# Performance work log

Hardware: AMD Instinct MI355X
Metric: run time of the kernel (lower is better)

Reference implementation:

```python
import jax, jax.numpy as jnp
import numpy as np

N_NODES = 200000
N_HYPEREDGES = 50000
NNZ = 3200000
D = 128
LEAKY = 0.2


def setup_inputs() -> dict:
    key = jax.random.key(0)
    k1, k2, k3, k4 = jax.random.split(key, 4)
    embs = jax.random.normal(k1, (N_NODES, D), dtype=jnp.float32)
    vals = jax.random.uniform(k2, (NNZ,), dtype=jnp.float32)
    rows = jax.random.randint(k3, (NNZ,), 0, N_NODES, dtype=jnp.int32)
    cols = jax.random.randint(k4, (NNZ,), 0, N_HYPEREDGES, dtype=jnp.int32)
    return {
        "embs": embs,
        "vals": vals,
        "rows": rows,
        "cols": cols,
        "n_nodes": N_NODES,
        "n_hyperedges": N_HYPEREDGES,
    }


def reference(embs, vals, rows, cols, n_nodes, n_hyperedges):
    # adj is sparse COO: adj[rows[k], cols[k]] = vals[k], shape [n_nodes, n_hyperedges]
    # Step 1: he = adj.T @ embs  -> [n_hyperedges, D]
    he = jax.ops.segment_sum(embs[rows] * vals[:, None], cols,
                             num_segments=n_hyperedges)
    # Step 2: out = adj @ he     -> [n_nodes, D]
    out = jax.ops.segment_sum(he[cols] * vals[:, None], rows,
                              num_segments=n_nodes)
    # LeakyReLU(negative_slope=LEAKY)
    return jnp.where(out >= 0, out, LEAKY * out)
```

## Files before the change

kernel.cpp:

```cpp
#include <hip/hip_runtime.h>

#define DIM 128
#define LEAKY 0.2f
#define N_NODES_C 200000
#define N_HE_C 50000

#define NNZ_SLAB 2048
#define SEGC_PB 64
#define NB_C 782
#define SEGR_PB 256
#define NB_R 782
#define CAP_B 4608

typedef float f32x4 __attribute__((ext_vector_type(4)));

__device__ __forceinline__ unsigned bf16r(float f) {
    return (__float_as_uint(f) + 0x8000u) >> 16;
}
__device__ __forceinline__ float bf16lo(unsigned u) {
    return __uint_as_float((u & 0xFFFFu) << 16);
}
__device__ __forceinline__ float bf16hi(unsigned u) {
    return __uint_as_float(u & 0xFFFF0000u);
}

__global__ void convert_bf16(const f32x4* __restrict__ in, uint2* __restrict__ out, int n4) {
    int t = blockIdx.x * blockDim.x + threadIdx.x;
    if (t >= n4) return;
    f32x4 x = __builtin_nontemporal_load(in + t);
    out[t] = make_uint2((bf16r(x.y) << 16) | bf16r(x.x),
                        (bf16r(x.w) << 16) | bf16r(x.z));
}

__global__ void __launch_bounds__(256)
bin_append(const int* __restrict__ rows, const int* __restrict__ cols,
           const float* __restrict__ vals, int nnz,
           int* __restrict__ curC, int* __restrict__ curR,
           int2* __restrict__ stagC, int2* __restrict__ stagR) {
    __shared__ int sr[NNZ_SLAB];
    __shared__ int sc[NNZ_SLAB];
    __shared__ int sv[NNZ_SLAB];
    __shared__ int cnt[NB_C + NB_R];
    for (int i = threadIdx.x; i < NB_C + NB_R; i += 256) cnt[i] = 0;
    __syncthreads();
    int base = blockIdx.x * NNZ_SLAB;
    int nloc = nnz - base; if (nloc > NNZ_SLAB) nloc = NNZ_SLAB;
    for (int i = threadIdx.x; i < nloc; i += 256) {
        int k = base + i;
        int r = rows[k], c = cols[k];
        sr[i] = r; sc[i] = c; sv[i] = __float_as_int(vals[k]);
        atomicAdd(&cnt[c >> 6], 1);
        atomicAdd(&cnt[NB_C + (r >> 8)], 1);
    }
    __syncthreads();
    for (int i = threadIdx.x; i < NB_C; i += 256) {
        int n = cnt[i];
        cnt[i] = n ? atomicAdd(&curC[i], n) : 0;
    }
    for (int i = threadIdx.x; i < NB_R; i += 256) {
        int n = cnt[NB_C + i];
        cnt[NB_C + i] = n ? atomicAdd(&curR[i], n) : 0;
    }
    __syncthreads();
    for (int i = threadIdx.x; i < nloc; i += 256) {
        int r = sr[i], c = sc[i], v = sv[i];
        int bc = c >> 6;
        int oc = atomicAdd(&cnt[bc], 1);
        if (oc < CAP_B)
            stagC[(size_t)bc * CAP_B + oc] = make_int2(((c & 63) << 18) | r, v);
        int br = r >> 8;
        int orr = atomicAdd(&cnt[NB_C + br], 1);
        if (orr < CAP_B)
            stagR[(size_t)br * CAP_B + orr] = make_int2(((r & 255) << 16) | c, v);
    }
}

template <int SEG_PB, int LSHIFT, int MODE>
__global__ void __launch_bounds__(256)
bucket_sort(const int* __restrict__ cur, const int2* __restrict__ stag,
            unsigned* __restrict__ outPacked,
            int* __restrict__ startOut, int* __restrict__ endOut, int nseg) {
    __shared__ int2 ent[CAP_B];
    __shared__ int cnt[SEG_PB];
    __shared__ int scn[SEG_PB];
    int b = blockIdx.x;
    size_t lo = (size_t)b * CAP_B;
    int n = cur[b]; if (n > CAP_B) n = CAP_B;
    int t = threadIdx.x;
    for (int i = t; i < SEG_PB; i += 256) cnt[i] = 0;
    __syncthreads();
    for (int i = t; i < n; i += 256) {
        int2 e = stag[lo + i];
        ent[i] = e;
        atomicAdd(&cnt[e.x >> LSHIFT], 1);
    }
    __syncthreads();
    if (t < SEG_PB) scn[t] = cnt[t];
    __syncthreads();
    for (int off = 1; off < SEG_PB; off <<= 1) {
        int x = (t < SEG_PB) ? scn[t] : 0;
        int add = (t >= off && t < SEG_PB) ? scn[t - off] : 0;
        __syncthreads();
        if (t < SEG_PB) scn[t] = x + add;
        __syncthreads();
    }
    int segBase = b * SEG_PB;
    if (t < SEG_PB) {
        int excl = t ? scn[t - 1] : 0;
        if (segBase + t < nseg) {
            startOut[segBase + t] = (int)lo + excl;
            endOut[segBase + t]   = (int)lo + scn[t];
        }
        cnt[t] = excl;
    }
    __syncthreads();
    for (int i = t; i < n; i += 256) {
        int2 e = ent[i];
        int s = e.x >> LSHIFT;
        int pos = (int)lo + atomicAdd(&cnt[s], 1);
        unsigned w;
        if (MODE == 0) {
            unsigned v14 = ((unsigned)e.y + 0x10000u) >> 17;
            w = ((unsigned)(e.x & 0x3FFFF) << 14) | (v14 & 0x3FFFu);
        } else {
            unsigned vb = ((unsigned)e.y + 0x8000u) >> 16;
            w = ((unsigned)(e.x & 0xFFFF) << 16) | vb;
        }
        outPacked[pos] = w;
    }
}


__global__ void seg_pass1(const int* __restrict__ start, const int* __restrict__ end,
                          const unsigned* __restrict__ packed,
                          const unsigned* __restrict__ srcb, unsigned* __restrict__ dstb,
                          int nseg) {
    int wid = (int)((blockIdx.x * (unsigned)blockDim.x + threadIdx.x) >> 6);
    int lane = threadIdx.x & 63;
    if (wid >= nseg) return;
    int s = start[wid];
    int e = end[wid];
    float ax = 0.f, ay = 0.f;
    int j = s;
    for (; j + 8 <= e; j += 8) {
        #pragma unroll
        for (int u = 0; u < 8; ++u) {
            unsigned p = packed[j + u];
            unsigned w = srcb[(size_t)(p >> 14) * 64 + lane];
            float v = __uint_as_float((p & 0x3FFFu) << 17);
            ax += bf16lo(w) * v;
            ay += bf16hi(w) * v;
        }
    }
    for (; j < e; ++j) {
        unsigned p = packed[j];
        unsigned w = srcb[(size_t)(p >> 14) * 64 + lane];
        float v = __uint_as_float((p & 0x3FFFu) << 17);
        ax += bf16lo(w) * v;
        ay += bf16hi(w) * v;
    }
    dstb[(size_t)wid * 64 + lane] = (bf16r(ay) << 16) | bf16r(ax);
}

__global__ void seg_pass2(const int* __restrict__ start, const int* __restrict__ end,
                          const unsigned* __restrict__ packed,
                          const unsigned* __restrict__ srcb, float* __restrict__ dst,
                          int nseg) {
    int wid = (int)((blockIdx.x * (unsigned)blockDim.x + threadIdx.x) >> 6);
    int lane = threadIdx.x & 63;
    if (wid >= nseg) return;
    int s = start[wid];
    int e = end[wid];
    float ax = 0.f, ay = 0.f;
    int j = s;
    for (; j + 4 <= e; j += 4) {
        #pragma unroll
        for (int u = 0; u < 4; ++u) {
            unsigned p = packed[j + u];
            unsigned w = srcb[(size_t)(p >> 16) * 64 + lane];
            float v = __uint_as_float(p << 16);
            ax += bf16lo(w) * v;
            ay += bf16hi(w) * v;
        }
    }
    for (; j < e; ++j) {
        unsigned p = packed[j];
        unsigned w = srcb[(size_t)(p >> 16) * 64 + lane];
        float v = __uint_as_float(p << 16);
        ax += bf16lo(w) * v;
        ay += bf16hi(w) * v;
    }
    ax = ax >= 0.f ? ax : LEAKY * ax;
    ay = ay >= 0.f ? ay : LEAKY * ay;
    unsigned long long bits = ((unsigned long long)__float_as_uint(ay) << 32) |
                              (unsigned long long)__float_as_uint(ax);
    __builtin_nontemporal_store(bits,
        reinterpret_cast<unsigned long long*>(dst) + (size_t)wid * 64 + lane);
}

__global__ void scatter_step(const float* __restrict__ src, const float* __restrict__ vals,
                             const int* __restrict__ gidx, const int* __restrict__ sidx,
                             float* __restrict__ dst, int nnz) {
    long long t = (long long)blockIdx.x * blockDim.x + threadIdx.x;
    int k = (int)(t >> 5);
    if (k >= nnz) return;
    int q = ((int)t & 31) << 2;
    int g = gidx[k];
    int s = sidx[k];
    float v = vals[k];
    const float4 e = *reinterpret_cast<const float4*>(src + (size_t)g * DIM + q);
    float* dp = dst + (size_t)s * DIM + q;
    unsafeAtomicAdd(dp + 0, e.x * v);
    unsafeAtomicAdd(dp + 1, e.y * v);
    unsafeAtomicAdd(dp + 2, e.z * v);
    unsafeAtomicAdd(dp + 3, e.w * v);
}

__global__ void leaky_inplace(float* __restrict__ out, int n4) {
    int t = blockIdx.x * blockDim.x + threadIdx.x;
    if (t >= n4) return;
    float4* p = reinterpret_cast<float4*>(out) + t;
    float4 x = *p;
    x.x = x.x >= 0.f ? x.x : LEAKY * x.x;
    x.y = x.y >= 0.f ? x.y : LEAKY * x.y;
    x.z = x.z >= 0.f ? x.z : LEAKY * x.z;
    x.w = x.w >= 0.f ? x.w : LEAKY * x.w;
    *p = x;
}

extern "C" void kernel_launch(void* const* d_in, const int* in_sizes, int n_in,
                              void* d_out, int out_size, void* d_ws, size_t ws_size,
                              hipStream_t stream) {
    const float* embs = (const float*)d_in[0];
    const float* vals = (const float*)d_in[1];
    const int*   rows = (const int*)d_in[2];
    const int*   cols = (const int*)d_in[3];
    const int nnz = in_sizes[1];
    float* out = (float*)d_out;

    unsigned* embsB = (unsigned*)d_out;

    char* ws = (char*)d_ws;
    size_t off = 0;
    auto alloc = [&](size_t bytes) -> char* {
        char* p = ws + off;
        off = (off + bytes + 255) & ~(size_t)255;
        return p;
    };
    unsigned* heB   = (unsigned*)alloc((size_t)N_HE_C * DIM * 2);
    int* startC     = (int*)alloc((size_t)N_HE_C * sizeof(int));
    int* endC       = (int*)alloc((size_t)N_HE_C * sizeof(int));
    int* startR     = (int*)alloc((size_t)N_NODES_C * sizeof(int));
    int* endR       = (int*)alloc((size_t)N_NODES_C * sizeof(int));
    int* curC       = (int*)alloc((size_t)NB_C * sizeof(int));
    int* curR       = (int*)alloc((size_t)NB_R * sizeof(int));
    int2* stagC     = (int2*)alloc((size_t)NB_C * CAP_B * sizeof(int2));
    int2* stagR     = (int2*)alloc((size_t)NB_R * CAP_B * sizeof(int2));
    size_t required = off;

    if (ws_size < required) {
        float* he = (float*)d_ws;
        (void)hipMemsetAsync(he,  0, (size_t)N_HE_C * DIM * sizeof(float), stream);
        (void)hipMemsetAsync(out, 0, (size_t)N_NODES_C * DIM * sizeof(float), stream);
        long long nthreads = (long long)nnz * 32;
        dim3 grd((unsigned)((nthreads + 255) / 256));
        scatter_step<<<grd, 256, 0, stream>>>(embs, vals, rows, cols, he, nnz);
        scatter_step<<<grd, 256, 0, stream>>>(he, vals, cols, rows, out, nnz);
        int n4 = N_NODES_C * DIM / 4;
        leaky_inplace<<<(n4 + 255) / 256, 256, 0, stream>>>(out, n4);
        return;
    }

    (void)hipMemsetAsync(curC, 0, (size_t)NB_C * sizeof(int), stream);
    (void)hipMemsetAsync(curR, 0, (size_t)NB_R * sizeof(int), stream);

    int nslab = (nnz + NNZ_SLAB - 1) / NNZ_SLAB;
    bin_append<<<nslab, 256, 0, stream>>>(rows, cols, vals, nnz,
                                          curC, curR, stagC, stagR);

    bucket_sort<SEGC_PB, 18, 0><<<NB_C, 256, 0, stream>>>(
        curC, stagC, (unsigned*)stagC, startC, endC, N_HE_C);
    bucket_sort<SEGR_PB, 16, 1><<<NB_R, 256, 0, stream>>>(
        curR, stagR, (unsigned*)stagR, startR, endR, N_NODES_C);

    {
        int n4 = N_NODES_C * DIM / 4;
        convert_bf16<<<(n4 + 255) / 256, 256, 0, stream>>>(
            (const f32x4*)embs, (uint2*)embsB, n4);
    }

    seg_pass1<<<(N_HE_C + 3) / 4, 256, 0, stream>>>(
        startC, endC, (const unsigned*)stagC, embsB, heB, N_HE_C);
    seg_pass2<<<(N_NODES_C + 3) / 4, 256, 0, stream>>>(
        startR, endR, (const unsigned*)stagR, heB, out, N_NODES_C);
}
```

Baseline: 432.7 us.

## Split node aggregation into four column-slice launches with sub-wave nnz parallelism

The second segment-sum pass now runs as four launches, each covering a 16-word slice of the bf16 hyperedge rows. Within a wave, four 16-lane groups process different nonzeros and are combined with cross-lane shuffles before the LeakyReLU and store. The idea is to shrink the gathered working set of each launch so it fits better in cache, and to increase memory-level parallelism per segment. In exchange, the packed index stream is read four times, there are extra launches, and each store covers only a quarter of a row.

```diff
diff --git a/kernel.cpp b/kernel.cpp
--- a/kernel.cpp
+++ b/kernel.cpp
@@ -162,40 +162,38 @@
     dstb[(size_t)wid * 64 + lane] = (bf16r(ay) << 16) | bf16r(ax);
 }
 
-__global__ void seg_pass2(const int* __restrict__ start, const int* __restrict__ end,
-                          const unsigned* __restrict__ packed,
-                          const unsigned* __restrict__ srcb, float* __restrict__ dst,
-                          int nseg) {
+__global__ void seg_pass2s(const int* __restrict__ start, const int* __restrict__ end,
+                           const unsigned* __restrict__ packed,
+                           const unsigned* __restrict__ srcb, float* __restrict__ dst,
+                           int nseg, int slice) {
     int wid = (int)((blockIdx.x * (unsigned)blockDim.x + threadIdx.x) >> 6);
     int lane = threadIdx.x & 63;
     if (wid >= nseg) return;
+    int g = lane >> 4;
+    int l = lane & 15;
     int s = start[wid];
     int e = end[wid];
+    const unsigned* src = srcb + slice * 16 + l;
     float ax = 0.f, ay = 0.f;
-    int j = s;
-    for (; j + 4 <= e; j += 4) {
-        #pragma unroll
-        for (int u = 0; u < 4; ++u) {
-            unsigned p = packed[j + u];
-            unsigned w = srcb[(size_t)(p >> 16) * 64 + lane];
-            float v = __uint_as_float(p << 16);
-            ax += bf16lo(w) * v;
-            ay += bf16hi(w) * v;
-        }
-    }
-    for (; j < e; ++j) {
+    for (int j = s + g; j < e; j += 4) {
         unsigned p = packed[j];
-        unsigned w = srcb[(size_t)(p >> 16) * 64 + lane];
+        unsigned w = src[(size_t)(p >> 16) * 64];
         float v = __uint_as_float(p << 16);
         ax += bf16lo(w) * v;
         ay += bf16hi(w) * v;
     }
-    ax = ax >= 0.f ? ax : LEAKY * ax;
-    ay = ay >= 0.f ? ay : LEAKY * ay;
-    unsigned long long bits = ((unsigned long long)__float_as_uint(ay) << 32) |
-                              (unsigned long long)__float_as_uint(ax);
-    __builtin_nontemporal_store(bits,
-        reinterpret_cast<unsigned long long*>(dst) + (size_t)wid * 64 + lane);
+    ax += __shfl_xor(ax, 16, 64);
+    ay += __shfl_xor(ay, 16, 64);
+    ax += __shfl_xor(ax, 32, 64);
+    ay += __shfl_xor(ay, 32, 64);
+    if (g == 0) {
+        ax = ax >= 0.f ? ax : LEAKY * ax;
+        ay = ay >= 0.f ? ay : LEAKY * ay;
+        unsigned long long bits = ((unsigned long long)__float_as_uint(ay) << 32) |
+                                  (unsigned long long)__float_as_uint(ax);
+        __builtin_nontemporal_store(bits,
+            reinterpret_cast<unsigned long long*>(dst) + (size_t)wid * 64 + slice * 16 + l);
+    }
 }
 
 __global__ void scatter_step(const float* __restrict__ src, const float* __restrict__ vals,
@@ -291,6 +289,9 @@
 
     seg_pass1<<<(N_HE_C + 3) / 4, 256, 0, stream>>>(
         startC, endC, (const unsigned*)stagC, embsB, heB, N_HE_C);
-    seg_pass2<<<(N_NODES_C + 3) / 4, 256, 0, stream>>>(
-        startR, endR, (const unsigned*)stagR, heB, out, N_NODES_C);
-}
+
+    for (int sl = 0; sl < 4; ++sl) {
+        seg_pass2s<<<(N_NODES_C + 3) / 4, 256, 0, stream>>>(
+            startR, endR, (const unsigned*)stagR, heB, out, N_NODES_C, sl);
+    }
+}
```

New measurement: 686.0 us. 1.59x slower.
